# Kernel optimization log

Measured on AMD Instinct MI355X. Metric: run time of the kernel, lower is better.

Reference implementation:

```python
import jax, jax.numpy as jnp
import numpy as np

B, T, C, J = 2048, 128, 3, 25   # batch, frames, coords, joints
E = 64                          # structure elements (n_elements)


def setup_inputs() -> dict:
    key = jax.random.key(0)
    k1, k2 = jax.random.split(key)
    x = jax.random.normal(k1, (B, T, C, J), dtype=jnp.float32)
    centres = jax.random.uniform(k2, (E, 2), dtype=jnp.float32)
    sharpness = jnp.full((E, 2), 3.0, dtype=jnp.float32)  # torch init: ones*3
    return {"x": x, "centres": centres, "sharpness": sharpness}


def _mst_deaths(Dm):
    """Prim's MST over dense distance matrix Dm [n,n].
    The multiset of MST edge weights equals the finite death times of the
    0-dim Vietoris-Rips persistence diagram (births are all 0)."""
    n = Dm.shape[0]
    in_tree0 = jnp.zeros(n, dtype=bool).at[0].set(True)

    def step(carry, _):
        mind, in_tree = carry
        masked = jnp.where(in_tree, jnp.inf, mind)  # distance from tree to each node
        j = jnp.argmin(masked)
        w = masked[j]                               # weight of edge added to MST
        in_tree = in_tree.at[j].set(True)
        mind = jnp.minimum(mind, Dm[j])
        return (mind, in_tree), w

    (_, _), deaths = jax.lax.scan(step, (Dm[0], in_tree0), None, length=n - 1)
    return deaths  # [n-1]


def reference(x, centres, sharpness):
    # --- dense preprocessing ---
    h = x.mean(1)                           # [B, C, J]
    h = h[..., :, None] - h[..., None, :]   # [B, C, J, J] pairwise coord diffs
    h = h.mean(-3)                          # [B, J, J]
    h = jnp.sqrt((h * h).sum(axis=1))       # torch.norm(., 2, dim=1) -> [B, J]
    lo, hi = h.min(), h.max()
    rng = hi - lo
    safe = rng > 1e-8
    h = jnp.where(safe, (h - lo) / jnp.where(safe, rng, 1.0), jnp.zeros_like(h))

    # --- Vietoris-Rips dim-0 persistence on point cloud h: B points in J dims ---
    sq = (h * h).sum(-1)
    d2 = sq[:, None] + sq[None, :] - 2.0 * (h @ h.T)       # [B, B]
    Dm = jnp.sqrt(jnp.maximum(d2, 1e-12))
    deaths = _mst_deaths(Dm)                               # [B-1]
    pd = jnp.stack([jnp.zeros_like(deaths), deaths], -1)[None]  # [1, P, 2]

    # --- StructureElementLayer: out[b,e] = sum_p exp(-sum_d s[e,d]^2 (pd-c)^2) ---
    s2 = sharpness * sharpness                             # [E, 2]
    diff = pd[:, :, None, :] - centres[None, None, :, :]   # [1, P, E, 2]
    out = jnp.exp(-(diff * diff * s2).sum(-1)).sum(1)      # [1, E]
    return out
```

## Files before the change

kernel.cpp:

```cpp
#include <hip/hip_runtime.h>
#include <math.h>

#define B_N 2048
#define T_N 128
#define C_N 3
#define J_N 25
#define E_N 64
#define TC  (T_N*C_N)
#define TCJ (TC*J_N)
#define NQ4 (TCJ/4)
#define NC  256

#define D_OFF      0
#define H_OFF      (B_N*B_N)
#define BLO_OFF    (H_OFF + B_N*J_N)
#define BHI_OFF    (BLO_OFF + B_N)
#define DEATHS_OFF (BHI_OFF + B_N)
#define BEST_OFF   (DEATHS_OFF + B_N)
#define COMP_OFF   (BEST_OFF + 4*B_N)
#define GC_OFF     (COMP_OFF + 2*B_N)
#define DC_OFF     (GC_OFF + 2)

typedef unsigned long long u64;
#define U64MAX 0xFFFFFFFFFFFFFFFFull
#define U32INF 0xFFFFFFFFu

__global__ void __launch_bounds__(256) k_reduce(const float* __restrict__ x,
                                                float* __restrict__ ws) {
    __shared__ float4 part[250];
    __shared__ float S[100];
    __shared__ float Mj[25];
    const int t = threadIdx.x, b = blockIdx.x;
    const float4* x4 = (const float4*)(x + (size_t)b * TCJ);
    if (t < 250) {
        float4 a; a.x = a.y = a.z = a.w = 0.f;
        for (int idx = t; idx < NQ4; idx += 250) {
            float4 v = x4[idx];
            a.x += v.x; a.y += v.y; a.z += v.z; a.w += v.w;
        }
        part[t] = a;
    }
    __syncthreads();
    if (t < 25) {
        float4 s = part[t];
        #pragma unroll
        for (int g = 1; g < 10; ++g) {
            float4 v = part[t + 25 * g];
            s.x += v.x; s.y += v.y; s.z += v.z; s.w += v.w;
        }
        S[4*t] = s.x; S[4*t+1] = s.y; S[4*t+2] = s.z; S[4*t+3] = s.w;
    }
    __syncthreads();
    if (t < 25) Mj[t] = (S[t] + S[t+25] + S[t+50] + S[t+75]) * (1.0f / 384.0f);
    __syncthreads();
    if (t < 25) {
        float mj = Mj[t], acc = 0.f;
        #pragma unroll
        for (int i = 0; i < J_N; ++i) { float d = Mj[i] - mj; acc += d * d; }
        float hv = sqrtf(acc);
        ws[H_OFF + b * J_N + t] = hv;
        S[t] = hv;
    }
    __syncthreads();
    if (t == 0) {
        float lo = S[0], hi = S[0];
        #pragma unroll
        for (int i = 1; i < J_N; ++i) { lo = fminf(lo, S[i]); hi = fmaxf(hi, S[i]); }
        ws[BLO_OFF + b] = lo;
        ws[BHI_OFF + b] = hi;
    }
}

__global__ void __launch_bounds__(1024) k_distscan(float* __restrict__ ws) {
    __shared__ float A[16][26];
    __shared__ float Bsh[1024 * J_N];
    const int t = threadIdx.x, blk = blockIdx.x;
    const int ty = t >> 6, tx = t & 63;
    const float* h = ws + H_OFF;
    const int row0 = blk * 16;
    for (int idx = t; idx < 16 * J_N; idx += 1024)
        A[idx / J_N][idx % J_N] = h[(row0 + idx / J_N) * J_N + idx % J_N];
    if (blk < 64) ((unsigned*)(ws + DC_OFF))[blk * 1024 + t] = U32INF;
    if (blk == 0) {
        unsigned* gc = (unsigned*)(ws + COMP_OFF);
        gc[t] = (unsigned)t; gc[t + 1024] = (unsigned)(t + 1024);
        if (t == 0) { ((unsigned*)(ws + GC_OFF))[0] = 0u; ((unsigned*)(ws + GC_OFF))[1] = 0u; }
    }
    const int row = row0 + ty;
    float ar[J_N];
    u64 bestk = U64MAX;
    float* D = ws + D_OFF;
    for (int mt = 0; mt < 2; ++mt) {
        __syncthreads();
        for (int idx = t; idx < 1024 * J_N; idx += 1024)
            Bsh[idx] = h[mt * 1024 * J_N + idx];
        __syncthreads();
        if (mt == 0) {
            #pragma unroll
            for (int k = 0; k < J_N; ++k) ar[k] = A[ty][k];
        }
        #pragma unroll 4
        for (int cc = 0; cc < 16; ++cc) {
            const int col = mt * 1024 + cc * 64 + tx;
            const float* bp = &Bsh[(cc * 64 + tx) * J_N];
            float acc = 0.f;
            #pragma unroll
            for (int k = 0; k < J_N; ++k) { float d = ar[k] - bp[k]; acc += d * d; }
            float dist = sqrtf(fmaxf(acc, 1e-12f));
            D[(size_t)row * B_N + col] = dist;
            if (col != row) {
                unsigned a = min((unsigned)row, (unsigned)col);
                unsigned b2 = max((unsigned)row, (unsigned)col);
                u64 key = ((u64)__float_as_uint(dist) << 32) | (a << 11) | b2;
                if (key < bestk) bestk = key;
            }
        }
    }
    #pragma unroll
    for (int off = 32; off; off >>= 1) {
        u64 o = __shfl_down(bestk, off);
        if (o < bestk) bestk = o;
    }
    if (tx == 0) ((u64*)(ws + BEST_OFF))[row] = bestk;
}

__global__ void __launch_bounds__(1024) k_round(float* __restrict__ ws, int par_in) {
    unsigned* gcnt = (unsigned*)(ws + GC_OFF);
    const unsigned base = gcnt[par_in];
    if (base >= B_N - 1) return;
    __shared__ __align__(16) unsigned comp[B_N];
    __shared__ u64 cb[B_N];
    __shared__ unsigned par[B_N];
    __shared__ unsigned cnt_s;
    const int t = threadIdx.x, blk = blockIdx.x;
    const unsigned* gcomp_in = (const unsigned*)(ws + COMP_OFF) + par_in * B_N;
    unsigned* gcomp_out = (unsigned*)(ws + COMP_OFF) + (par_in ^ 1) * B_N;
    const u64* bin = (const u64*)(ws + BEST_OFF) + par_in * B_N;
    u64* bout = (u64*)(ws + BEST_OFF) + (par_in ^ 1) * B_N;
    float* deaths = ws + DEATHS_OFF;

    if (t == 0) cnt_s = 0u;
    comp[t] = gcomp_in[t]; comp[t + 1024] = gcomp_in[t + 1024];
    cb[t] = U64MAX; cb[t + 1024] = U64MAX;
    __syncthreads();
    #pragma unroll
    for (int i = t; i < B_N; i += 1024) {
        u64 bk = bin[i];
        if (bk != U64MAX) atomicMin(&cb[comp[i]], bk);
    }
    __syncthreads();
    #pragma unroll
    for (int c = t; c < B_N; c += 1024) {
        u64 k = cb[c];
        unsigned p = (unsigned)c;
        if (k != U64MAX) {
            unsigned a  = (unsigned)((k >> 11) & 0x7FFu);
            unsigned b2 = (unsigned)(k & 0x7FFu);
            unsigned ca = comp[a], cbv = comp[b2];
            unsigned c2 = (ca == (unsigned)c) ? cbv : ca;
            p = c2;
            if (!(cb[c2] == k && c2 < (unsigned)c)) {
                unsigned li = atomicAdd(&cnt_s, 1u);
                if (blk == 0) deaths[base + li] = __uint_as_float((unsigned)(k >> 32));
            }
        }
        par[c] = p;
    }
    __syncthreads();
    #pragma unroll
    for (int c = t; c < B_N; c += 1024) {
        unsigned p = par[c];
        if (p != (unsigned)c && par[p] == (unsigned)c && (unsigned)c < p) par[c] = (unsigned)c;
    }
    __syncthreads();
    #pragma unroll
    for (int c = t; c < B_N; c += 1024) {
        unsigned r = par[c];
        while (true) { unsigned pr = par[r]; if (pr == r) break; r = pr; }
        par[c] = r;
    }
    __syncthreads();
    #pragma unroll
    for (int i = t; i < B_N; i += 1024) comp[i] = par[comp[i]];
    __syncthreads();
    const unsigned newbase = base + cnt_s;
    if (blk == 0) {
        gcomp_out[t] = comp[t]; gcomp_out[t + 1024] = comp[t + 1024];
        if (t == 0) { gcnt[par_in ^ 1] = newbase; if (newbase >= B_N - 1) gcnt[par_in] = newbase; }
    }
    if (newbase >= B_N - 1) return;

    const int w = t >> 6, lane = t & 63;
    const int row = blk * 16 + w;
    const unsigned ci = comp[row];
    u64 prev = bin[row];
    {
        unsigned pa = (unsigned)((prev >> 11) & 0x7FFu);
        unsigned pb = (unsigned)(prev & 0x7FFu);
        unsigned jo = (pa == (unsigned)row) ? pb : pa;
        if (comp[jo] != ci) {
            if (lane == 0) bout[row] = prev;
            return;
        }
    }
    const float4* row4 = (const float4*)(ws + D_OFF + (size_t)row * B_N);
    const uint4* comp4 = (const uint4*)comp;
    u64 best = U64MAX;
    #pragma unroll
    for (int k = 0; k < 8; ++k) {
        const int q = k * 64 + lane;
        float4 w4 = row4[q];
        uint4  c4 = comp4[q];
        const unsigned j0 = (unsigned)(q * 4);
        float wv[4] = {w4.x, w4.y, w4.z, w4.w};
        unsigned cv[4] = {c4.x, c4.y, c4.z, c4.w};
        #pragma unroll
        for (int m = 0; m < 4; ++m) {
            if (cv[m] != ci) {
                unsigned j = j0 + m;
                unsigned a = min((unsigned)row, j), b2 = max((unsigned)row, j);
                u64 key = ((u64)__float_as_uint(wv[m]) << 32) | (a << 11) | b2;
                if (key < best) best = key;
            }
        }
    }
    #pragma unroll
    for (int off = 32; off; off >>= 1) {
        u64 o = __shfl_down(best, off);
        if (o < best) best = o;
    }
    if (lane == 0) bout[row] = best;
}

__global__ void __launch_bounds__(1024) k_round3c(float* __restrict__ ws) {
    unsigned* gcnt = (unsigned*)(ws + GC_OFF);
    const unsigned base = gcnt[0];
    if (base >= B_N - 1) return;
    __shared__ __align__(16) unsigned comp[B_N];
    __shared__ u64 cb[B_N];
    __shared__ unsigned par[B_N];
    __shared__ unsigned cflag[B_N];
    __shared__ unsigned pd[16][NC];
    __shared__ unsigned cnt_s, csum[16];
    const int t = threadIdx.x, blk = blockIdx.x;
    const unsigned* gcomp_in = (const unsigned*)(ws + COMP_OFF);
    const u64* bin = (const u64*)(ws + BEST_OFF);
    float* deaths = ws + DEATHS_OFF;

    if (t == 0) cnt_s = 0u;
    comp[t] = gcomp_in[t]; comp[t + 1024] = gcomp_in[t + 1024];
    cb[t] = U64MAX; cb[t + 1024] = U64MAX;
    __syncthreads();
    #pragma unroll
    for (int i = t; i < B_N; i += 1024) {
        u64 bk = bin[i];
        if (bk != U64MAX) atomicMin(&cb[comp[i]], bk);
    }
    __syncthreads();
    #pragma unroll
    for (int c = t; c < B_N; c += 1024) {
        u64 k = cb[c];
        unsigned p = (unsigned)c;
        if (k != U64MAX) {
            unsigned a  = (unsigned)((k >> 11) & 0x7FFu);
            unsigned b2 = (unsigned)(k & 0x7FFu);
            unsigned ca = comp[a], cbv = comp[b2];
            unsigned c2 = (ca == (unsigned)c) ? cbv : ca;
            p = c2;
            if (!(cb[c2] == k && c2 < (unsigned)c)) {
                unsigned li = atomicAdd(&cnt_s, 1u);
                if (blk == 0) deaths[base + li] = __uint_as_float((unsigned)(k >> 32));
            }
        }
        par[c] = p;
    }
    __syncthreads();
    #pragma unroll
    for (int c = t; c < B_N; c += 1024) {
        unsigned p = par[c];
        if (p != (unsigned)c && par[p] == (unsigned)c && (unsigned)c < p) par[c] = (unsigned)c;
    }
    __syncthreads();
    #pragma unroll
    for (int c = t; c < B_N; c += 1024) {
        unsigned r = par[c];
        while (true) { unsigned pr = par[r]; if (pr == r) break; r = pr; }
        par[c] = r;
    }
    __syncthreads();
    #pragma unroll
    for (int i = t; i < B_N; i += 1024) comp[i] = par[comp[i]];
    __syncthreads();
    const unsigned newbase = base + cnt_s;
    if (blk == 0 && t == 0) { gcnt[0] = newbase; gcnt[1] = newbase; }
    if (newbase >= B_N - 1) return;

    cflag[t] = 0u; cflag[t + 1024] = 0u;
    __syncthreads();
    cflag[comp[t]] = 1u; cflag[comp[t + 1024]] = 1u;
    __syncthreads();
    const unsigned lane = t & 63, w = t >> 6;
    unsigned f0 = cflag[2 * t], f1 = cflag[2 * t + 1];
    unsigned s = f0 + f1, sc = s;
    #pragma unroll
    for (int off = 1; off < 64; off <<= 1) {
        unsigned v = __shfl_up(sc, off);
        if (lane >= (unsigned)off) sc += v;
    }
    if (lane == 63) csum[w] = sc;
    __syncthreads();
    if (t < 16) {
        unsigned v = csum[t], acc = v;
        #pragma unroll
        for (int off = 1; off < 16; off <<= 1) {
            unsigned u2 = __shfl_up(acc, off);
            if (t >= off) acc += u2;
        }
        csum[t] = acc - v;
    }
    __syncthreads();
    unsigned off0 = csum[w] + (sc - s);
    __syncthreads();
    if (f0) cflag[2 * t] = off0;
    if (f1) cflag[2 * t + 1] = off0 + f0;
    __syncthreads();

    #pragma unroll
    for (int i = 0; i < 4; ++i) pd[0][i * 1024 + t] = U32INF;
    __syncthreads();
    const int row = blk * 16 + (int)w;
    const unsigned ci = comp[row];
    {
        const float4* row4 = (const float4*)(ws + D_OFF + (size_t)row * B_N);
        const uint4* comp4 = (const uint4*)comp;
        #pragma unroll
        for (int k = 0; k < 8; ++k) {
            const int q = k * 64 + (int)lane;
            float4 w4 = row4[q];
            uint4  c4 = comp4[q];
            float wv[4] = {w4.x, w4.y, w4.z, w4.w};
            unsigned cv[4] = {c4.x, c4.y, c4.z, c4.w};
            #pragma unroll
            for (int m = 0; m < 4; ++m) {
                if (cv[m] != ci) atomicMin(&pd[w][cflag[cv[m]]], __float_as_uint(wv[m]));
            }
        }
    }
    __syncthreads();
    unsigned* gDc = (unsigned*)(ws + DC_OFF);
    const unsigned ri = cflag[ci];
    for (int j2 = (int)lane; j2 < NC; j2 += 64) {
        unsigned v = pd[w][j2];
        if (v != U32INF) atomicMin(&gDc[ri * NC + j2], v);
    }
}

__global__ void __launch_bounds__(1024) k_finishstruct(float* __restrict__ ws,
                                                       const float* __restrict__ centres,
                                                       const float* __restrict__ sharp,
                                                       float* __restrict__ out) {
    __shared__ unsigned short Dcs[NC * NC];
    __shared__ u64 cbf[NC];
    __shared__ unsigned parf[NC], ccomp[NC];
    __shared__ unsigned cnt_s, base_s;
    __shared__ float redlo[16], redhi[16];
    const int t = threadIdx.x;
    const int lane = t & 63, w = t >> 6;
    float* deaths = ws + DEATHS_OFF;
    const unsigned base0 = ((const unsigned*)(ws + GC_OFF))[0];

    if (base0 < B_N - 1) {
        const unsigned* gDc = (const unsigned*)(ws + DC_OFF);
        #pragma unroll
        for (int i = 0; i < 64; ++i) {
            unsigned v = gDc[i * 1024 + t];
            Dcs[i * 1024 + t] = (unsigned short)(v >> 16);
        }
        if (t < NC) ccomp[t] = (unsigned)t;
        if (t == 0) base_s = base0;
        __syncthreads();
        for (int iter = 0; iter < 8; ++iter) {
            if (t < NC) cbf[t] = U64MAX;
            if (t == 0) cnt_s = 0u;
            __syncthreads();
            #pragma unroll
            for (int q = 0; q < 16; ++q) {
                const int r = w * 16 + q;
                const unsigned cc = ccomp[r];
                u64 key = U64MAX;
                #pragma unroll
                for (int hh = 0; hh < 4; ++hh) {
                    const int c = lane + hh * 64;
                    unsigned wv = Dcs[r * NC + c];
                    if (wv != 0xFFFFu && ccomp[c] != cc) {
                        unsigned a = min((unsigned)r, (unsigned)c);
                        unsigned b2 = max((unsigned)r, (unsigned)c);
                        u64 k2 = ((u64)wv << 32) | (a << 8) | b2;
                        if (k2 < key) key = k2;
                    }
                }
                #pragma unroll
                for (int off = 32; off; off >>= 1) {
                    u64 o = __shfl_down(key, off);
                    if (o < key) key = o;
                }
                if (lane == 0 && key != U64MAX) atomicMin(&cbf[cc], key);
            }
            __syncthreads();
            bool add = false; float dw = 0.f;
            if (t < NC) {
                u64 k = cbf[t];
                unsigned p = (unsigned)t;
                if (k != U64MAX) {
                    unsigned a = (unsigned)((k >> 8) & 255u), b2 = (unsigned)(k & 255u);
                    unsigned ca = ccomp[a], cbv = ccomp[b2];
                    unsigned c2 = (ca == (unsigned)t) ? cbv : ca;
                    p = c2;
                    if (!(cbf[c2] == k && c2 < (unsigned)t)) {
                        add = true;
                        dw = __uint_as_float((unsigned)(k >> 32) << 16);
                    }
                }
                parf[t] = p;
            }
            __syncthreads();
            if (t < NC) {
                unsigned pp = parf[t];
                if (pp != (unsigned)t && parf[pp] == (unsigned)t && (unsigned)t < pp) parf[t] = (unsigned)t;
            }
            __syncthreads();
            if (t < NC) {
                unsigned r2 = parf[t];
                while (parf[r2] != r2) r2 = parf[r2];
                parf[t] = r2;
            }
            __syncthreads();
            if (t < NC) {
                if (add) { unsigned li = atomicAdd(&cnt_s, 1u); deaths[base_s + li] = dw; }
                ccomp[t] = parf[ccomp[t]];
            }
            __syncthreads();
            if (t == 0) base_s += cnt_s;
            __syncthreads();
            if (base_s >= B_N - 1) break;
        }
        __syncthreads();
    }

    float lo = INFINITY, hi = -INFINITY;
    #pragma unroll
    for (int i = t; i < B_N; i += 1024) {
        lo = fminf(lo, ws[BLO_OFF + i]);
        hi = fmaxf(hi, ws[BHI_OFF + i]);
    }
    #pragma unroll
    for (int off = 32; off; off >>= 1) {
        lo = fminf(lo, __shfl_down(lo, off));
        hi = fmaxf(hi, __shfl_down(hi, off));
    }
    if (lane == 0) { redlo[w] = lo; redhi[w] = hi; }
    __syncthreads();
    lo = redlo[0]; hi = redhi[0];
    #pragma unroll
    for (int k = 1; k < 16; ++k) { lo = fminf(lo, redlo[k]); hi = fmaxf(hi, redhi[k]); }
    float rng = hi - lo;
    float rinv = (rng > 1e-8f) ? 1.0f / rng : 0.0f;

    for (int e = w; e < E_N; e += 16) {
        const float c0 = centres[e * 2], c1 = centres[e * 2 + 1];
        const float s0 = sharp[e * 2],   s1 = sharp[e * 2 + 1];
        const float s1sq = s1 * s1;
        float acc = 0.f;
        for (int p = lane; p < B_N - 1; p += 64) {
            float d = deaths[p] * rinv - c1;
            acc += expf(-s1sq * d * d);
        }
        #pragma unroll
        for (int off = 32; off; off >>= 1) acc += __shfl_down(acc, off);
        if (lane == 0) out[e] = expf(-s0 * s0 * c0 * c0) * acc;
    }
}

extern "C" void kernel_launch(void* const* d_in, const int* in_sizes, int n_in,
                              void* d_out, int out_size, void* d_ws, size_t ws_size,
                              hipStream_t stream) {
    const float* x       = (const float*)d_in[0];
    const float* centres = (const float*)d_in[1];
    const float* sharp   = (const float*)d_in[2];
    float* out = (float*)d_out;
    float* ws  = (float*)d_ws;

    hipLaunchKernelGGL(k_reduce,   dim3(B_N),  dim3(256),  0, stream, x, ws);
    hipLaunchKernelGGL(k_distscan, dim3(128),  dim3(1024), 0, stream, ws);
    hipLaunchKernelGGL(k_round,    dim3(128),  dim3(1024), 0, stream, ws, 0);
    hipLaunchKernelGGL(k_round,    dim3(128),  dim3(1024), 0, stream, ws, 1);
    hipLaunchKernelGGL(k_round3c,  dim3(128),  dim3(1024), 0, stream, ws);
    hipLaunchKernelGGL(k_finishstruct, dim3(1), dim3(1024), 0, stream, ws, centres, sharp, out);
}
```

Baseline: 178.8 us.

## Fuse third Boruvka round with finishing kernel via last-block ticket

Merges the round-3 contraction kernel and the single-block finish/structure-element kernel into one launch. A global ticket counter lets the last block to finish run the compressed-graph MST and output stage, which removes one kernel launch and its gap. Death writes now go to deterministic slots from a prefix scan instead of atomic order, and shared memory is overlaid in one arena. The cost is a larger shared-memory footprint per block, which may lower occupancy, plus extra fence and atomic overhead.

```diff
diff --git a/kernel.cpp b/kernel.cpp
--- a/kernel.cpp
+++ b/kernel.cpp
@@ -19,7 +19,8 @@
 #define BEST_OFF   (DEATHS_OFF + B_N)
 #define COMP_OFF   (BEST_OFF + 4*B_N)
 #define GC_OFF     (COMP_OFF + 2*B_N)
-#define DC_OFF     (GC_OFF + 2)
+#define TK_OFF     (GC_OFF + 2)
+#define DC_OFF     (GC_OFF + 4)
 
 typedef unsigned long long u64;
 #define U64MAX 0xFFFFFFFFFFFFFFFFull
@@ -84,7 +85,11 @@
     if (blk == 0) {
         unsigned* gc = (unsigned*)(ws + COMP_OFF);
         gc[t] = (unsigned)t; gc[t + 1024] = (unsigned)(t + 1024);
-        if (t == 0) { ((unsigned*)(ws + GC_OFF))[0] = 0u; ((unsigned*)(ws + GC_OFF))[1] = 0u; }
+        if (t == 0) {
+            ((unsigned*)(ws + GC_OFF))[0] = 0u;
+            ((unsigned*)(ws + GC_OFF))[1] = 0u;
+            *(unsigned*)(ws + TK_OFF) = 0u;
+        }
     }
     const int row = row0 + ty;
     float ar[J_N];
@@ -232,152 +237,190 @@
     if (lane == 0) bout[row] = best;
 }
 
-__global__ void __launch_bounds__(1024) k_round3c(float* __restrict__ ws) {
+__global__ void __launch_bounds__(1024) k_round3cf(float* __restrict__ ws,
+                                                   const float* __restrict__ centres,
+                                                   const float* __restrict__ sharp,
+                                                   float* __restrict__ out) {
+    __shared__ __align__(16) unsigned char arena[135168];
+    __shared__ unsigned cnt_s, csum[16], lastflag, base_s;
+    __shared__ float redlo[16], redhi[16];
+    unsigned* comp  = (unsigned*)arena;
+    u64*      cb    = (u64*)(arena + 8192);
+    unsigned* par   = (unsigned*)(arena + 24576);
+    unsigned* cflag = (unsigned*)(arena + 32768);
+    unsigned* pd    = (unsigned*)(arena + 40960);
+    unsigned* af    = (unsigned*)(arena + 57344);
+    float*    dwv   = (float*)(arena + 65536);
+    unsigned short* Dcs = (unsigned short*)arena;
+    u64*      cbf   = (u64*)(arena + 131072);
+    unsigned* parf  = (unsigned*)(arena + 133120);
+    unsigned* ccomp = (unsigned*)(arena + 134144);
+
+    const int t = threadIdx.x, blk = blockIdx.x;
+    const unsigned lane = t & 63, w = t >> 6;
     unsigned* gcnt = (unsigned*)(ws + GC_OFF);
+    float* deaths = ws + DEATHS_OFF;
+    unsigned* gDc = (unsigned*)(ws + DC_OFF);
     const unsigned base = gcnt[0];
-    if (base >= B_N - 1) return;
-    __shared__ __align__(16) unsigned comp[B_N];
-    __shared__ u64 cb[B_N];
-    __shared__ unsigned par[B_N];
-    __shared__ unsigned cflag[B_N];
-    __shared__ unsigned pd[16][NC];
-    __shared__ unsigned cnt_s, csum[16];
-    const int t = threadIdx.x, blk = blockIdx.x;
-    const unsigned* gcomp_in = (const unsigned*)(ws + COMP_OFF);
-    const u64* bin = (const u64*)(ws + BEST_OFF);
-    float* deaths = ws + DEATHS_OFF;
-
-    if (t == 0) cnt_s = 0u;
-    comp[t] = gcomp_in[t]; comp[t + 1024] = gcomp_in[t + 1024];
-    cb[t] = U64MAX; cb[t + 1024] = U64MAX;
-    __syncthreads();
-    #pragma unroll
-    for (int i = t; i < B_N; i += 1024) {
-        u64 bk = bin[i];
-        if (bk != U64MAX) atomicMin(&cb[comp[i]], bk);
-    }
-    __syncthreads();
-    #pragma unroll
-    for (int c = t; c < B_N; c += 1024) {
-        u64 k = cb[c];
-        unsigned p = (unsigned)c;
-        if (k != U64MAX) {
-            unsigned a  = (unsigned)((k >> 11) & 0x7FFu);
-            unsigned b2 = (unsigned)(k & 0x7FFu);
-            unsigned ca = comp[a], cbv = comp[b2];
-            unsigned c2 = (ca == (unsigned)c) ? cbv : ca;
-            p = c2;
-            if (!(cb[c2] == k && c2 < (unsigned)c)) {
-                unsigned li = atomicAdd(&cnt_s, 1u);
-                if (blk == 0) deaths[base + li] = __uint_as_float((unsigned)(k >> 32));
-            }
-        }
-        par[c] = p;
-    }
-    __syncthreads();
-    #pragma unroll
-    for (int c = t; c < B_N; c += 1024) {
-        unsigned p = par[c];
-        if (p != (unsigned)c && par[p] == (unsigned)c && (unsigned)c < p) par[c] = (unsigned)c;
-    }
-    __syncthreads();
-    #pragma unroll
-    for (int c = t; c < B_N; c += 1024) {
-        unsigned r = par[c];
-        while (true) { unsigned pr = par[r]; if (pr == r) break; r = pr; }
-        par[c] = r;
-    }
-    __syncthreads();
-    #pragma unroll
-    for (int i = t; i < B_N; i += 1024) comp[i] = par[comp[i]];
-    __syncthreads();
-    const unsigned newbase = base + cnt_s;
-    if (blk == 0 && t == 0) { gcnt[0] = newbase; gcnt[1] = newbase; }
-    if (newbase >= B_N - 1) return;
-
-    cflag[t] = 0u; cflag[t + 1024] = 0u;
-    __syncthreads();
-    cflag[comp[t]] = 1u; cflag[comp[t + 1024]] = 1u;
-    __syncthreads();
-    const unsigned lane = t & 63, w = t >> 6;
-    unsigned f0 = cflag[2 * t], f1 = cflag[2 * t + 1];
-    unsigned s = f0 + f1, sc = s;
-    #pragma unroll
-    for (int off = 1; off < 64; off <<= 1) {
-        unsigned v = __shfl_up(sc, off);
-        if (lane >= (unsigned)off) sc += v;
-    }
-    if (lane == 63) csum[w] = sc;
-    __syncthreads();
-    if (t < 16) {
-        unsigned v = csum[t], acc = v;
-        #pragma unroll
-        for (int off = 1; off < 16; off <<= 1) {
-            unsigned u2 = __shfl_up(acc, off);
-            if (t >= off) acc += u2;
-        }
-        csum[t] = acc - v;
-    }
-    __syncthreads();
-    unsigned off0 = csum[w] + (sc - s);
-    __syncthreads();
-    if (f0) cflag[2 * t] = off0;
-    if (f1) cflag[2 * t + 1] = off0 + f0;
-    __syncthreads();
-
-    #pragma unroll
-    for (int i = 0; i < 4; ++i) pd[0][i * 1024 + t] = U32INF;
-    __syncthreads();
-    const int row = blk * 16 + (int)w;
-    const unsigned ci = comp[row];
-    {
-        const float4* row4 = (const float4*)(ws + D_OFF + (size_t)row * B_N);
-        const uint4* comp4 = (const uint4*)comp;
-        #pragma unroll
-        for (int k = 0; k < 8; ++k) {
-            const int q = k * 64 + (int)lane;
-            float4 w4 = row4[q];
-            uint4  c4 = comp4[q];
-            float wv[4] = {w4.x, w4.y, w4.z, w4.w};
-            unsigned cv[4] = {c4.x, c4.y, c4.z, c4.w};
+    unsigned newbase = base;
+
+    if (base < B_N - 1) {
+        const unsigned* gcomp_in = (const unsigned*)(ws + COMP_OFF);
+        const u64* bin = (const u64*)(ws + BEST_OFF);
+        if (t == 0) cnt_s = 0u;
+        comp[t] = gcomp_in[t]; comp[t + 1024] = gcomp_in[t + 1024];
+        cb[t] = U64MAX; cb[t + 1024] = U64MAX;
+        __syncthreads();
+        #pragma unroll
+        for (int i = t; i < B_N; i += 1024) {
+            u64 bk = bin[i];
+            if (bk != U64MAX) atomicMin(&cb[comp[i]], bk);
+        }
+        __syncthreads();
+        #pragma unroll
+        for (int c = t; c < B_N; c += 1024) {
+            u64 k = cb[c];
+            unsigned p = (unsigned)c, flag = 0u;
+            float dw = 0.f;
+            if (k != U64MAX) {
+                unsigned a  = (unsigned)((k >> 11) & 0x7FFu);
+                unsigned b2 = (unsigned)(k & 0x7FFu);
+                unsigned ca = comp[a], cbv = comp[b2];
+                unsigned c2 = (ca == (unsigned)c) ? cbv : ca;
+                p = c2;
+                if (!(cb[c2] == k && c2 < (unsigned)c)) {
+                    flag = 1u; dw = __uint_as_float((unsigned)(k >> 32));
+                    atomicAdd(&cnt_s, 1u);
+                }
+            }
+            par[c] = p; af[c] = flag; dwv[c] = dw;
+        }
+        __syncthreads();
+        #pragma unroll
+        for (int c = t; c < B_N; c += 1024) {
+            unsigned p = par[c];
+            if (p != (unsigned)c && par[p] == (unsigned)c && (unsigned)c < p) par[c] = (unsigned)c;
+        }
+        __syncthreads();
+        #pragma unroll
+        for (int c = t; c < B_N; c += 1024) {
+            unsigned r = par[c];
+            while (true) { unsigned pr = par[r]; if (pr == r) break; r = pr; }
+            par[c] = r;
+        }
+        __syncthreads();
+        #pragma unroll
+        for (int i = t; i < B_N; i += 1024) comp[i] = par[comp[i]];
+        unsigned f0 = af[2 * t], f1 = af[2 * t + 1];
+        unsigned s2 = f0 + f1, sc2 = s2;
+        #pragma unroll
+        for (int off = 1; off < 64; off <<= 1) {
+            unsigned v = __shfl_up(sc2, off);
+            if (lane >= (unsigned)off) sc2 += v;
+        }
+        if (lane == 63) csum[w] = sc2;
+        __syncthreads();
+        if (t < 16) {
+            unsigned v = csum[t], acc = v;
             #pragma unroll
-            for (int m = 0; m < 4; ++m) {
-                if (cv[m] != ci) atomicMin(&pd[w][cflag[cv[m]]], __float_as_uint(wv[m]));
-            }
-        }
-    }
-    __syncthreads();
-    unsigned* gDc = (unsigned*)(ws + DC_OFF);
-    const unsigned ri = cflag[ci];
-    for (int j2 = (int)lane; j2 < NC; j2 += 64) {
-        unsigned v = pd[w][j2];
-        if (v != U32INF) atomicMin(&gDc[ri * NC + j2], v);
-    }
-}
-
-__global__ void __launch_bounds__(1024) k_finishstruct(float* __restrict__ ws,
-                                                       const float* __restrict__ centres,
-                                                       const float* __restrict__ sharp,
-                                                       float* __restrict__ out) {
-    __shared__ unsigned short Dcs[NC * NC];
-    __shared__ u64 cbf[NC];
-    __shared__ unsigned parf[NC], ccomp[NC];
-    __shared__ unsigned cnt_s, base_s;
-    __shared__ float redlo[16], redhi[16];
-    const int t = threadIdx.x;
-    const int lane = t & 63, w = t >> 6;
-    float* deaths = ws + DEATHS_OFF;
-    const unsigned base0 = ((const unsigned*)(ws + GC_OFF))[0];
-
-    if (base0 < B_N - 1) {
-        const unsigned* gDc = (const unsigned*)(ws + DC_OFF);
+            for (int off = 1; off < 16; off <<= 1) {
+                unsigned u2 = __shfl_up(acc, off);
+                if (t >= off) acc += u2;
+            }
+            csum[t] = acc - v;
+        }
+        __syncthreads();
+        {
+            unsigned off0 = csum[w] + (sc2 - s2);
+            af[2 * t]     = f0 ? off0        : U32INF;
+            af[2 * t + 1] = f1 ? (off0 + f0) : U32INF;
+        }
+        __syncthreads();
+        #pragma unroll
+        for (int c = t; c < B_N; c += 1024) {
+            unsigned s = af[c];
+            if (s != U32INF) deaths[base + s] = dwv[c];
+        }
+        newbase = base + cnt_s;
+
+        if (newbase < B_N - 1) {
+            cflag[t] = 0u; cflag[t + 1024] = 0u;
+            __syncthreads();
+            cflag[comp[t]] = 1u; cflag[comp[t + 1024]] = 1u;
+            __syncthreads();
+            unsigned g0 = cflag[2 * t], g1 = cflag[2 * t + 1];
+            unsigned s3 = g0 + g1, sc3 = s3;
+            #pragma unroll
+            for (int off = 1; off < 64; off <<= 1) {
+                unsigned v = __shfl_up(sc3, off);
+                if (lane >= (unsigned)off) sc3 += v;
+            }
+            if (lane == 63) csum[w] = sc3;
+            __syncthreads();
+            if (t < 16) {
+                unsigned v = csum[t], acc = v;
+                #pragma unroll
+                for (int off = 1; off < 16; off <<= 1) {
+                    unsigned u2 = __shfl_up(acc, off);
+                    if (t >= off) acc += u2;
+                }
+                csum[t] = acc - v;
+            }
+            __syncthreads();
+            {
+                unsigned off0 = csum[w] + (sc3 - s3);
+                if (g0) cflag[2 * t] = off0;
+                if (g1) cflag[2 * t + 1] = off0 + g0;
+            }
+            __syncthreads();
+            #pragma unroll
+            for (int i = 0; i < 4; ++i) pd[i * 1024 + t] = U32INF;
+            __syncthreads();
+            const int row = blk * 16 + (int)w;
+            const unsigned ci = comp[row];
+            {
+                const float4* row4 = (const float4*)(ws + D_OFF + (size_t)row * B_N);
+                const uint4* comp4 = (const uint4*)comp;
+                #pragma unroll
+                for (int k = 0; k < 8; ++k) {
+                    const int q = k * 64 + (int)lane;
+                    float4 w4 = row4[q];
+                    uint4  c4 = comp4[q];
+                    float wv[4] = {w4.x, w4.y, w4.z, w4.w};
+                    unsigned cv[4] = {c4.x, c4.y, c4.z, c4.w};
+                    #pragma unroll
+                    for (int m = 0; m < 4; ++m) {
+                        if (cv[m] != ci) atomicMin(&pd[w * NC + cflag[cv[m]]], __float_as_uint(wv[m]));
+                    }
+                }
+            }
+            __syncthreads();
+            const unsigned ri = cflag[ci];
+            for (int j2 = (int)lane; j2 < NC; j2 += 64) {
+                unsigned v = pd[w * NC + j2];
+                if (v != U32INF) atomicMin(&gDc[ri * NC + j2], v);
+            }
+        }
+    }
+
+    __syncthreads();
+    if (t == 0) {
+        __threadfence();
+        unsigned prev = atomicAdd((unsigned*)(ws + TK_OFF), 1u);
+        lastflag = (prev == gridDim.x - 1) ? 1u : 0u;
+    }
+    __syncthreads();
+    if (!lastflag) return;
+
+    if (newbase < B_N - 1) {
         #pragma unroll
         for (int i = 0; i < 64; ++i) {
-            unsigned v = gDc[i * 1024 + t];
+            unsigned v = __hip_atomic_load(&gDc[i * 1024 + t], __ATOMIC_RELAXED,
+                                           __HIP_MEMORY_SCOPE_AGENT);
             Dcs[i * 1024 + t] = (unsigned short)(v >> 16);
         }
         if (t < NC) ccomp[t] = (unsigned)t;
-        if (t == 0) base_s = base0;
+        if (t == 0) base_s = newbase;
         __syncthreads();
         for (int iter = 0; iter < 8; ++iter) {
             if (t < NC) cbf[t] = U64MAX;
@@ -385,12 +428,12 @@
             __syncthreads();
             #pragma unroll
             for (int q = 0; q < 16; ++q) {
-                const int r = w * 16 + q;
+                const int r = (int)w * 16 + q;
                 const unsigned cc = ccomp[r];
                 u64 key = U64MAX;
                 #pragma unroll
                 for (int hh = 0; hh < 4; ++hh) {
-                    const int c = lane + hh * 64;
+                    const int c = (int)lane + hh * 64;
                     unsigned wv = Dcs[r * NC + c];
                     if (wv != 0xFFFFu && ccomp[c] != cc) {
                         unsigned a = min((unsigned)r, (unsigned)c);
@@ -466,12 +509,12 @@
     float rng = hi - lo;
     float rinv = (rng > 1e-8f) ? 1.0f / rng : 0.0f;
 
-    for (int e = w; e < E_N; e += 16) {
+    for (int e = (int)w; e < E_N; e += 16) {
         const float c0 = centres[e * 2], c1 = centres[e * 2 + 1];
         const float s0 = sharp[e * 2],   s1 = sharp[e * 2 + 1];
         const float s1sq = s1 * s1;
         float acc = 0.f;
-        for (int p = lane; p < B_N - 1; p += 64) {
+        for (int p = (int)lane; p < B_N - 1; p += 64) {
             float d = deaths[p] * rinv - c1;
             acc += expf(-s1sq * d * d);
         }
@@ -494,6 +537,5 @@
     hipLaunchKernelGGL(k_distscan, dim3(128),  dim3(1024), 0, stream, ws);
     hipLaunchKernelGGL(k_round,    dim3(128),  dim3(1024), 0, stream, ws, 0);
     hipLaunchKernelGGL(k_round,    dim3(128),  dim3(1024), 0, stream, ws, 1);
-    hipLaunchKernelGGL(k_round3c,  dim3(128),  dim3(1024), 0, stream, ws);
-    hipLaunchKernelGGL(k_finishstruct, dim3(1), dim3(1024), 0, stream, ws, centres, sharp, out);
+    hipLaunchKernelGGL(k_round3cf, dim3(128),  dim3(1024), 0, stream, ws, centres, sharp, out);
 }
```

Result: no change. 179.2 us (+0.2%).
